# Optimization experiments

Measured on AMD Instinct MI355X. Metric: run time of the kernel, lower is better.

The kernel has to match this reference:

```python
import jax, jax.numpy as jnp
import numpy as np

B, T_ENC, T_DEC = 32, 300, 500
N_MEL, ENC_DIM, ATT_RNN, DEC_RNN, PRE = 80, 512, 1024, 1024, 256
ATT_DIM, LOC_F, LOC_K = 128, 32, 31
PAD = (LOC_K - 1) // 2
P_PRENET = 0.1


def _w(k, shape, fan_in):
    return jax.random.normal(k, shape, jnp.float32) / np.float32(np.sqrt(fan_in))


def setup_inputs() -> dict:
    key = jax.random.key(0)
    ks = jax.random.split(key, 20)
    lens = jax.random.randint(ks[2], (B,), T_ENC // 2, T_ENC + 1).at[0].set(T_ENC)
    return {
        "memory": jax.random.normal(ks[0], (B, T_ENC, ENC_DIM), jnp.float32),
        "decoder_inputs": jax.random.normal(ks[1], (B, N_MEL, T_DEC), jnp.float32),
        "memory_lengths": lens,
        "pre_W1": _w(ks[3], (PRE, N_MEL), N_MEL),
        "pre_W2": _w(ks[4], (PRE, PRE), PRE),
        "att_Wih": _w(ks[5], (4 * ATT_RNN, PRE + ENC_DIM), PRE + ENC_DIM),
        "att_Whh": _w(ks[6], (4 * ATT_RNN, ATT_RNN), ATT_RNN),
        "att_bih": jnp.zeros((4 * ATT_RNN,), jnp.float32),
        "att_bhh": jnp.zeros((4 * ATT_RNN,), jnp.float32),
        "q_W": _w(ks[7], (ATT_DIM, ATT_RNN), ATT_RNN),
        "m_W": _w(ks[8], (ATT_DIM, ENC_DIM), ENC_DIM),
        "v_w": _w(ks[9], (ATT_DIM,), ATT_DIM),
        "loc_conv_W": _w(ks[10], (LOC_F, 2, LOC_K), 2 * LOC_K),
        "loc_dense_W": _w(ks[11], (ATT_DIM, LOC_F), LOC_F),
        "dec_Wih": _w(ks[12], (4 * DEC_RNN, ATT_RNN + ENC_DIM), ATT_RNN + ENC_DIM),
        "dec_Whh": _w(ks[13], (4 * DEC_RNN, DEC_RNN), DEC_RNN),
        "dec_bih": jnp.zeros((4 * DEC_RNN,), jnp.float32),
        "dec_bhh": jnp.zeros((4 * DEC_RNN,), jnp.float32),
        "proj_W": _w(ks[14], (N_MEL, DEC_RNN + ENC_DIM), DEC_RNN + ENC_DIM),
        "proj_b": jnp.zeros((N_MEL,), jnp.float32),
        "gate_W": _w(ks[15], (DEC_RNN + ENC_DIM,), DEC_RNN + ENC_DIM),
        "gate_b": jnp.zeros((), jnp.float32),
    }


def _lstm(x, h, c, Wih, Whh, bih, bhh):
    # PyTorch LSTMCell gate order: i, f, g, o
    g = x @ Wih.T + bih + h @ Whh.T + bhh
    i, f, gg, o = jnp.split(g, 4, axis=-1)
    c = jax.nn.sigmoid(f) * c + jax.nn.sigmoid(i) * jnp.tanh(gg)
    h = jax.nn.sigmoid(o) * jnp.tanh(c)
    return h, c


def _prenet(x, W1, W2):
    # Original uses F.dropout(..., 0.1, training=True) always; deterministic masks here.
    k1, k2 = jax.random.split(jax.random.key(1))
    x = jax.nn.relu(x @ W1.T)
    x = x * jax.random.bernoulli(k1, 1.0 - P_PRENET, x.shape) / (1.0 - P_PRENET)
    x = jax.nn.relu(x @ W2.T)
    x = x * jax.random.bernoulli(k2, 1.0 - P_PRENET, x.shape) / (1.0 - P_PRENET)
    return x


def _forward(memory, decoder_inputs, memory_lengths, pre_W1, pre_W2, att_Wih, att_Whh,
             att_bih, att_bhh, q_W, m_W, v_w, loc_conv_W, loc_dense_W, dec_Wih, dec_Whh,
             dec_bih, dec_bhh, proj_W, proj_b, gate_W, gate_b):
    x = jnp.transpose(decoder_inputs, (2, 0, 1))          # [T_dec, B, n_mel]
    go = jnp.zeros((1,) + x.shape[1:], x.dtype)
    x = jnp.concatenate([go, x], axis=0)                  # [T_dec+1, B, n_mel]
    dec_ins = _prenet(x, pre_W1, pre_W2)[:-1]             # [T_dec, B, PRE]

    processed_memory = memory @ m_W.T                     # [B, T_enc, ATT_DIM]
    valid = jnp.arange(T_ENC)[None, :] < memory_lengths[:, None]  # [B, T_enc]
    Bn = memory.shape[0]
    zf = lambda d: jnp.zeros((Bn, d), memory.dtype)
    carry0 = (zf(ATT_RNN), zf(ATT_RNN), zf(DEC_RNN), zf(DEC_RNN),
              zf(T_ENC), zf(T_ENC), zf(ENC_DIM))

    def step(carry, x_t):
        ah, ac, dh, dc, aw, awc, ctx = carry
        ah, ac = _lstm(jnp.concatenate([x_t, ctx], 1), ah, ac,
                       att_Wih, att_Whh, att_bih, att_bhh)
        awcat = jnp.stack([aw, awc], axis=1)              # [B, 2, T_enc]
        loc = jax.lax.conv_general_dilated(awcat, loc_conv_W, (1,), [(PAD, PAD)],
                                           dimension_numbers=('NCH', 'OIH', 'NCH'))
        loc = jnp.transpose(loc, (0, 2, 1)) @ loc_dense_W.T   # [B, T_enc, ATT_DIM]
        pq = (ah @ q_W.T)[:, None, :]                     # [B, 1, ATT_DIM]
        e = jnp.tanh(pq + loc + processed_memory) @ v_w   # [B, T_enc]
        e = jnp.where(valid, e, -jnp.inf)
        aw = jax.nn.softmax(e, axis=1)
        ctx = jnp.einsum('bt,btd->bd', aw, memory)        # [B, ENC_DIM]
        awc = awc + aw
        dh, dc = _lstm(jnp.concatenate([ah, ctx], 1), dh, dc,
                       dec_Wih, dec_Whh, dec_bih, dec_bhh)
        dhac = jnp.concatenate([dh, ctx], 1)
        mel = dhac @ proj_W.T + proj_b                    # [B, n_mel]
        gate = dhac @ gate_W + gate_b                     # [B]
        return (ah, ac, dh, dc, aw, awc, ctx), (mel, gate, aw)

    _, (mels, gates, aligns) = jax.lax.scan(jax.checkpoint(step), carry0, dec_ins)
    mel_outputs = jnp.transpose(mels, (1, 2, 0))          # [B, n_mel, T_dec]
    gate_outputs = gates.T                                # [B, T_dec]
    alignments = jnp.transpose(aligns, (1, 0, 2))         # [B, T_dec, T_enc]
    return mel_outputs, gate_outputs, alignments


def reference(memory, decoder_inputs, memory_lengths, pre_W1, pre_W2, att_Wih, att_Whh,
              att_bih, att_bhh, q_W, m_W, v_w, loc_conv_W, loc_dense_W, dec_Wih, dec_Whh,
              dec_bih, dec_bhh, proj_W, proj_b, gate_W, gate_b):
    return _forward(memory, decoder_inputs, memory_lengths, pre_W1, pre_W2, att_Wih,
                    att_Whh, att_bih, att_bhh, q_W, m_W, v_w, loc_conv_W, loc_dense_W,
                    dec_Wih, dec_Whh, dec_bih, dec_bhh, proj_W, proj_b, gate_W, gate_b)
```

## Files before the change

kernel.cpp:

```cpp
#include <hip/hip_runtime.h>

#define NB 32
#define TENC 300
#define TDEC 500
#define NMEL 80
#define ENCD 512
#define PRE 256
#define ADIM 128
#define RD 4
#define WSPLIT 2944

#define OFF_DECINS 0ull
#define OFF_WHI    2048000ull
#define OFF_AHR    4096000ull
#define OFF_DHR    (OFF_AHR + 131072ull)
#define OFF_CXR    (OFF_DHR + 131072ull)
#define RINGS_N    327680ull
#define OFF_WLO    (OFF_AHR + RINGS_N)
#define OFF_PM     8192000ull
#define OFF_STATE  (OFF_PM + 1228800ull)
#define OFF_AC     (OFF_STATE + 0ull)
#define OFF_DC     (OFF_STATE + 32768ull)
#define OFF_AW     (OFF_STATE + 65536ull)
#define OFF_AWC    (OFF_STATE + 75136ull)
#define OFF_E      (OFF_STATE + 84736ull)
#define OFF_SLOTS  (OFF_STATE + 94336ull)
#define STATE_N    98440ull
#define OFF_QWT    (OFF_STATE + STATE_N)
#define OFF_PROJWT (OFF_QWT + 131072ull)
#define OFF_MWT    (OFF_PROJWT + 122880ull)
#define OFF_W1T    (OFF_MWT + 65536ull)
#define OFF_W2T    (OFF_W1T + 20480ull)

__device__ __forceinline__ unsigned short f2bf(float f){
  unsigned u = __float_as_uint(f);
  unsigned r = (u + 0x7FFFu + ((u >> 16) & 1u)) >> 16;
  return (unsigned short)r;
}
__device__ __forceinline__ float bf2f(unsigned short h){
  return __uint_as_float(((unsigned)h) << 16);
}

__device__ __forceinline__ float gload(const float* p){
  return __hip_atomic_load(p, __ATOMIC_RELAXED, __HIP_MEMORY_SCOPE_AGENT);
}
__device__ __forceinline__ void gstore(float* p, float v){
  __hip_atomic_store(p, v, __ATOMIC_RELAXED, __HIP_MEMORY_SCOPE_AGENT);
}

__device__ __forceinline__ void gbar(unsigned* slots, unsigned epoch){
  __syncthreads();
  int tid = threadIdx.x;
  if (tid == 0)
    __hip_atomic_store(&slots[blockIdx.x], epoch, __ATOMIC_RELAXED, __HIP_MEMORY_SCOPE_AGENT);
  if (tid < 64){
    const unsigned long long* p = (const unsigned long long*)slots;
    unsigned long long a, b;
    do {
      a = __hip_atomic_load(p + 2*tid,     __ATOMIC_RELAXED, __HIP_MEMORY_SCOPE_AGENT);
      b = __hip_atomic_load(p + 2*tid + 1, __ATOMIC_RELAXED, __HIP_MEMORY_SCOPE_AGENT);
    } while ((unsigned)a < epoch || (unsigned)(a >> 32) < epoch ||
             (unsigned)b < epoch || (unsigned)(b >> 32) < epoch);
  }
  __syncthreads();
}

__host__ __device__ __forceinline__ unsigned rotl32(unsigned v, int r){ return (v<<r)|(v>>(32-r)); }

__host__ __device__ __forceinline__ void tf2x32(unsigned k0, unsigned k1, unsigned c0, unsigned c1,
                                                unsigned& y0, unsigned& y1){
  unsigned ks2 = k0 ^ k1 ^ 0x1BD11BDAu;
  unsigned x0 = c0 + k0, x1 = c1 + k1;
#define TFR(r) x0 += x1; x1 = rotl32(x1, r); x1 ^= x0;
  TFR(13) TFR(15) TFR(26) TFR(6)
  x0 += k1;  x1 += ks2 + 1u;
  TFR(17) TFR(29) TFR(16) TFR(24)
  x0 += ks2; x1 += k0 + 2u;
  TFR(13) TFR(15) TFR(26) TFR(6)
  x0 += k0;  x1 += k1 + 3u;
  TFR(17) TFR(29) TFR(16) TFR(24)
  x0 += k1;  x1 += ks2 + 4u;
  TFR(13) TFR(15) TFR(26) TFR(6)
  x0 += ks2; x1 += k0 + 5u;
#undef TFR
  y0 = x0; y1 = x1;
}

__device__ __forceinline__ float mask_scale(unsigned k0, unsigned k1, unsigned idx){
  unsigned y0, y1;
  tf2x32(k0, k1, 0u, idx, y0, y1);
  unsigned bits = y0 ^ y1;
  float u = __uint_as_float((bits >> 9) | 0x3f800000u) - 1.0f;
  return (u < 0.9f) ? (1.0f/0.9f) : 0.0f;
}

__global__ __launch_bounds__(256) void k_setup(float* __restrict__ ws,
    const float* __restrict__ qW, const float* __restrict__ projW, const float* __restrict__ mW,
    const float* __restrict__ w1, const float* __restrict__ w2,
    const float* __restrict__ dWih, const float* __restrict__ dWhh){
  long i = (long)blockIdx.x*256 + threadIdx.x;
  long stride = (long)gridDim.x*256;
  float* st = ws + OFF_STATE;
  for (long x = i; x < (long)STATE_N; x += stride) st[x] = 0.f;
  float* qWT = ws + OFF_QWT;
  for (long x = i; x < 1024*128; x += stride){ int u = x>>7, d = x&127; qWT[x] = qW[(size_t)d*1024+u]; }
  float* pWT = ws + OFF_PROJWT;
  for (long x = i; x < 1536*80; x += stride){ int k = x/80, m = x%80; pWT[x] = projW[(size_t)m*1536+k]; }
  float* mWT = ws + OFF_MWT;
  for (long x = i; x < 512*128; x += stride){ int k = x>>7, d = x&127; mWT[x] = mW[(size_t)d*512+k]; }
  float* w1T = ws + OFF_W1T;
  for (long x = i; x < 80*256; x += stride){ int m = x>>8, u = x&255; w1T[x] = w1[(size_t)u*80+m]; }
  float* w2T = ws + OFF_W2T;
  for (long x = i; x < 256*256; x += stride){ int k = x>>8, u = x&255; w2T[x] = w2[(size_t)u*256+k]; }
  unsigned short* wlo = (unsigned short*)(ws + OFF_WLO);
  for (long x = i; x < (long)WSPLIT*2560; x += stride){
    int row = (int)(x/2560), c = (int)(x%2560);
    float v = (c < 1536) ? dWih[(size_t)row*1536 + c] : dWhh[(size_t)row*1024 + (c-1536)];
    wlo[x] = f2bf(v);
  }
  unsigned short* whi = (unsigned short*)(ws + OFF_WHI);
  for (long x = i; x < (long)(4096-WSPLIT)*2560; x += stride){
    int row = WSPLIT + (int)(x/2560), c = (int)(x%2560);
    float v = (c < 1536) ? dWih[(size_t)row*1536 + c] : dWhh[(size_t)row*1024 + (c-1536)];
    whi[x] = f2bf(v);
  }
}

__global__ __launch_bounds__(256) void k_prenet(const float* __restrict__ di,
    const float* __restrict__ W1T, const float* __restrict__ W2T,
    unsigned short* __restrict__ dec_ins,
    unsigned k10, unsigned k11, unsigned k20, unsigned k21){
  __shared__ float xs[NMEL];
  __shared__ float h1s[PRE];
  int bid = blockIdx.x;
  int t = bid >> 5, b = bid & 31;
  int tid = threadIdx.x;
  if (tid < NMEL) xs[tid] = (t == 0) ? 0.f : di[(size_t)b*40000 + (size_t)tid*500 + (t-1)];
  __syncthreads();
  float acc = 0.f;
  for (int m = 0; m < NMEL; ++m) acc += xs[m] * W1T[m*256 + tid];
  acc = fmaxf(acc, 0.f);
  unsigned idx = (unsigned)bid*256u + (unsigned)tid;
  h1s[tid] = acc * mask_scale(k10, k11, idx);
  __syncthreads();
  float a2 = 0.f;
  for (int k = 0; k < PRE; ++k) a2 += h1s[k] * W2T[k*256 + tid];
  a2 = fmaxf(a2, 0.f);
  a2 *= mask_scale(k20, k21, idx);
  dec_ins[(size_t)bid*256 + tid] = f2bf(a2);
}

__global__ __launch_bounds__(128) void k_procmem(const float* __restrict__ mem,
    const float* __restrict__ mWT, float* __restrict__ pm){
  __shared__ float ms[ENCD];
  int bid = blockIdx.x;
  int tid = threadIdx.x;
  const float* src = mem + (size_t)bid*ENCD;
  for (int i = tid; i < ENCD; i += 128) ms[i] = src[i];
  __syncthreads();
  float acc = 0.f;
  for (int k = 0; k < ENCD; ++k) acc += ms[k] * mWT[k*128 + tid];
  pm[(size_t)bid*128 + tid] = acc;
}

template<bool S0B>
__device__ __forceinline__ float2 xld2(const void* s0v, int l0, const float* s1,
                                       const float* h, int b, int k){
  if (k < l0){
    if constexpr (S0B){
      const unsigned short* s0 = (const unsigned short*)s0v;
      unsigned u = *(const unsigned*)(s0 + (size_t)b*l0 + k);
      float2 r; r.x = __uint_as_float((u & 0xFFFFu) << 16); r.y = __uint_as_float((u >> 16) << 16);
      return r;
    } else {
      const float* s0 = (const float*)s0v;
      return *(const float2*)(s0 + (size_t)b*l0 + k);
    }
  }
  if (k < l0 + 512) return *(const float2*)(s1 + (b<<9) + (k - l0));
  return *(const float2*)(h + (b<<10) + (k - (l0 + 512)));
}

template<bool S0B, bool WB>
__device__ __forceinline__ void lstm_block(int ub,
    const float* __restrict__ W1, const float* __restrict__ W2,
    const unsigned short* __restrict__ wlo, const unsigned short* __restrict__ whi,
    const float* __restrict__ bih, const float* __restrict__ bhh,
    const void* __restrict__ s0, int l0, const float* __restrict__ s1,
    const float* __restrict__ hprev, int Ktot,
    float* __restrict__ c_st, float* __restrict__ hnew, int tid){
  __shared__ float Xc[2][128*32];
  __shared__ float gates[16][32];
  const int xw = l0 + 512, xw4 = xw >> 2;
  const int NC = Ktot >> 7;
  const int w = tid >> 6, l = tid & 63;
  const int ss = l & 31, ph = l >> 5;
  const int rlA = 2*w, rlB = 2*w + 1;
  const int rowA = (rlA >> 2)*1024 + ub*4 + (rlA & 3);
  const int rowB = (rlB >> 2)*1024 + ub*4 + (rlB & 3);
  const float4* W1A = (const float4*)(W1 + (size_t)rowA*xw);
  const float4* W1B = (const float4*)(W1 + (size_t)rowB*xw);
  const float4* W2A = (const float4*)(W2 + ((size_t)rowA<<10));
  const float4* W2B = (const float4*)(W2 + ((size_t)rowB<<10));
  const unsigned short* BA = nullptr; const unsigned short* BB = nullptr;
  if constexpr (WB){
    BA = (rowA < WSPLIT) ? wlo + (size_t)rowA*2560 : whi + (size_t)(rowA - WSPLIT)*2560;
    BB = (rowB < WSPLIT) ? wlo + (size_t)rowB*2560 : whi + (size_t)(rowB - WSPLIT)*2560;
  }
  auto loadWA = [&](int f)->float4{
    if constexpr (WB){
      ushort4 h4 = *(const ushort4*)(BA + 4*(size_t)f);
      return make_float4(bf2f(h4.x), bf2f(h4.y), bf2f(h4.z), bf2f(h4.w));
    } else return (f < xw4) ? W1A[f] : W2A[f - xw4];
  };
  auto loadWB = [&](int f)->float4{
    if constexpr (WB){
      ushort4 h4 = *(const ushort4*)(BB + 4*(size_t)f);
      return make_float4(bf2f(h4.x), bf2f(h4.y), bf2f(h4.z), bf2f(h4.w));
    } else return (f < xw4) ? W1B[f] : W2B[f - xw4];
  };
  float accA[16] = {}, accB[16] = {};
  float2 sx[4];
#pragma unroll
  for (int it = 0; it < 4; ++it){
    int pidx = tid + it*512;
    int b = pidx >> 6, kL = (pidx & 63)*2;
    sx[it] = xld2<S0B>(s0, l0, s1, hprev, b, kL);
  }
#pragma unroll
  for (int it = 0; it < 4; ++it){
    int pidx = tid + it*512;
    int b = pidx >> 6, kL = (pidx & 63)*2;
    int a0 = kL*32 + (((b>>2) ^ ((kL>>2)&7))<<2) + (b&3);
    Xc[0][a0] = sx[it].x; Xc[0][a0+32] = sx[it].y;
  }
  float4 wA = loadWA(ss), wB = loadWB(ss);
  __syncthreads();

  for (int c = 0; c < NC; ++c){
    float4 wAn, wBn;
    if (c + 1 < NC){
      int f = (c+1)*32 + ss;
      wAn = loadWA(f); wBn = loadWB(f);
      int kg0 = (c+1) << 7;
#pragma unroll
      for (int it = 0; it < 4; ++it){
        int pidx = tid + it*512;
        int b = pidx >> 6, kL = (pidx & 63)*2;
        sx[it] = xld2<S0B>(s0, l0, s1, hprev, b, kg0 + kL);
      }
    }
    const float4* X4 = (const float4*)Xc[c & 1];
    const int sw = ss & 7;
#pragma unroll
    for (int e = 0; e < 4; ++e){
      int kL = 4*ss + e;
      float ea = (e==0)?wA.x:(e==1)?wA.y:(e==2)?wA.z:wA.w;
      float eb = (e==0)?wB.x:(e==1)?wB.y:(e==2)?wB.z:wB.w;
      int base = kL*8;
#pragma unroll
      for (int j = 0; j < 4; ++j){
        int g = ph*4 + j;
        float4 xv = X4[base + (g ^ sw)];
        accA[4*j+0] += ea*xv.x; accA[4*j+1] += ea*xv.y;
        accA[4*j+2] += ea*xv.z; accA[4*j+3] += ea*xv.w;
        accB[4*j+0] += eb*xv.x; accB[4*j+1] += eb*xv.y;
        accB[4*j+2] += eb*xv.z; accB[4*j+3] += eb*xv.w;
      }
    }
    if (c + 1 < NC){
#pragma unroll
      for (int it = 0; it < 4; ++it){
        int pidx = tid + it*512;
        int b = pidx >> 6, kL = (pidx & 63)*2;
        int a0 = kL*32 + (((b>>2) ^ ((kL>>2)&7))<<2) + (b&3);
        Xc[(c+1)&1][a0] = sx[it].x; Xc[(c+1)&1][a0+32] = sx[it].y;
      }
      wA = wAn; wB = wBn;
    }
    __syncthreads();
  }
#pragma unroll
  for (int j = 0; j < 16; ++j){
    accA[j] += __shfl_xor(accA[j], 16, 64);
    accB[j] += __shfl_xor(accB[j], 16, 64);
  }
#pragma unroll
  for (int m = 8; m >= 1; m >>= 1){
    int up = ss & m;
#pragma unroll
    for (int j = 0; j < m; ++j){
      float sA = up ? accA[j] : accA[j+m];
      float kA = up ? accA[j+m] : accA[j];
      float sB = up ? accB[j] : accB[j+m];
      float kB = up ? accB[j+m] : accB[j];
      accA[j] = kA + __shfl_xor(sA, m, 64);
      accB[j] = kB + __shfl_xor(sB, m, 64);
    }
  }
  if (!(l & 16)){
    int b = ph*16 + (l & 15);
    gates[rlA][b] = accA[0];
    gates[rlB][b] = accB[0];
  }
  __syncthreads();
  if (tid < 128){
    int b = tid & 31, u = tid >> 5;
    int gu = ub*4 + u;
    float gi = gates[u][b]     + bih[gu]         + bhh[gu];
    float gf = gates[4+u][b]   + bih[1024+gu]    + bhh[1024+gu];
    float gg = gates[8+u][b]   + bih[2048+gu]    + bhh[2048+gu];
    float go = gates[12+u][b]  + bih[3072+gu]    + bhh[3072+gu];
    float ii = 1.f/(1.f + expf(-gi));
    float ff = 1.f/(1.f + expf(-gf));
    float oo = 1.f/(1.f + expf(-go));
    float tg = tanhf(gg);
    float cold = gload(&c_st[b*1024 + gu]);
    float cn = ff*cold + ii*tg;
    gstore(&c_st[b*1024 + gu], cn);
    gstore(&hnew[b*1024 + gu], oo*tanhf(cn));
  }
  __syncthreads();
}

__device__ __forceinline__ void energy_tile(int b, int tile, bool act, int h,
    const float* __restrict__ aw, const float* __restrict__ awc,
    const float* __restrict__ lcW, const float* __restrict__ ldW, const float* __restrict__ vw,
    const float* __restrict__ sPq, const float* __restrict__ pm, float* __restrict__ e_ws, int t2){
  __shared__ float sIn[2][2][46];
  __shared__ float cfs[2][16][33];
  __shared__ float ep[2][16][17];
  int j0 = tile*16;
  if (act){
    if (t2 < 46){ int j = j0 - 15 + t2; sIn[h][0][t2] = (j >= 0 && j < 300) ? gload(&aw[b*300 + j]) : 0.f; }
    else if (t2 < 92){ int i = t2 - 46; int j = j0 - 15 + i; sIn[h][1][i] = (j >= 0 && j < 300) ? gload(&awc[b*300 + j]) : 0.f; }
  }
  __syncthreads();
  if (act){
    int fg = t2 & 15, jl = t2 >> 4;
    int f0 = 2*fg;
    float c0 = 0.f, c1 = 0.f;
#pragma unroll
    for (int c = 0; c < 2; ++c)
#pragma unroll
      for (int k = 0; k < 31; ++k){
        float a = sIn[h][c][jl + k];
        c0 += a * lcW[f0*62 + c*31 + k];
        c1 += a * lcW[(f0+1)*62 + c*31 + k];
      }
    cfs[h][jl][f0] = c0; cfs[h][jl][f0+1] = c1;
  }
  __syncthreads();
  if (act){
    int dg = t2 & 15, jl = t2 >> 4;
    int j = j0 + jl;
    float s = 0.f;
    if (j < 300){
      const float* pmrow = pm + ((size_t)(b*300 + j))*128 + dg*8;
#pragma unroll
      for (int dd = 0; dd < 8; ++dd){
        int d = dg*8 + dd;
        float acc = sPq[d] + pmrow[dd];
#pragma unroll
        for (int f = 0; f < 32; ++f) acc += cfs[h][jl][f] * ldW[d*32 + f];
        s += vw[d] * tanhf(acc);
      }
    }
    ep[h][jl][dg] = s;
  }
  __syncthreads();
  if (act && t2 < 16){
    int j = j0 + t2;
    if (j < 300){
      float s = 0.f;
#pragma unroll
      for (int dg = 0; dg < 16; ++dg) s += ep[h][t2][dg];
      gstore(&e_ws[b*300 + j], s);
    }
  }
  __syncthreads();
}

__device__ __forceinline__ void pq_energy(int b, int jt, const float* __restrict__ ah,
    const float* __restrict__ qWT, const float* __restrict__ aw, const float* __restrict__ awc,
    const float* __restrict__ lcW, const float* __restrict__ ldW, const float* __restrict__ vw,
    const float* __restrict__ pm, float* __restrict__ e_ws, int tid){
  __shared__ float sAh[1024];
  __shared__ float pqs[512];
  __shared__ float sPq[128];
  for (int i = tid; i < 1024; i += 512) sAh[i] = ah[b*1024 + i];
  __syncthreads();
  int d = tid & 127, seg = tid >> 7;
  const float* qt = qWT + (size_t)(seg*256)*128 + d;
  const float* sh = sAh + seg*256;
  float a0 = 0.f, a1 = 0.f, a2 = 0.f, a3 = 0.f;
  for (int u = 0; u < 256; u += 4){
    a0 += sh[u]   * qt[(size_t)u*128];
    a1 += sh[u+1] * qt[(size_t)(u+1)*128];
    a2 += sh[u+2] * qt[(size_t)(u+2)*128];
    a3 += sh[u+3] * qt[(size_t)(u+3)*128];
  }
  pqs[seg*128 + d] = (a0 + a1) + (a2 + a3);
  __syncthreads();
  if (tid < 128) sPq[tid] = (pqs[tid] + pqs[128+tid]) + (pqs[256+tid] + pqs[384+tid]);
  __syncthreads();
  int h = tid >> 8, t2 = tid & 255;
  for (int r = 0; r < 2; ++r){
    int tile = r*16 + jt*2 + h;
    energy_tile(b, tile, tile < 19, h, aw, awc, lcW, ldW, vw, sPq, pm, e_ws, t2);
  }
}

__device__ __forceinline__ void dec_out_slice(int b, int jt,
    const float* __restrict__ dh, const float* __restrict__ ctx,
    const float* __restrict__ pWT, const float* __restrict__ projb,
    const float* __restrict__ gateW, const float* __restrict__ gateb,
    float* __restrict__ out, int s, int tid){
  __shared__ float sX[1536];
  __shared__ float melp[48][11];
  __shared__ float gatep[32];
  for (int i = tid; i < 1024; i += 512) sX[i] = dh[b*1024 + i];
  if (tid < 512) { int i = tid; sX[1024 + i] = ctx[b*512 + i]; }
  __syncthreads();
  if (tid < 480){
    int mi = tid % 10, kseg = tid / 10;
    int m = jt*10 + mi;
    const float* pw = pWT + m;
    int k0 = kseg*32;
    float a0 = 0.f, a1 = 0.f;
#pragma unroll 8
    for (int k = 0; k < 32; k += 2){
      a0 += sX[k0+k]   * pw[(size_t)(k0+k)*80];
      a1 += sX[k0+k+1] * pw[(size_t)(k0+k+1)*80];
    }
    melp[kseg][mi] = a0 + a1;
  } else if (jt == 0){
    int kseg = tid - 480;
    int k0 = kseg*48;
    float a = 0.f;
    for (int k = 0; k < 48; ++k) a += sX[k0+k] * gateW[k0+k];
    gatep[kseg] = a;
  }
  __syncthreads();
  if (tid < 10){
    float s2 = projb[jt*10 + tid];
    for (int q = 0; q < 48; ++q) s2 += melp[q][tid];
    out[(size_t)b*40000 + (size_t)(jt*10 + tid)*500 + s] = s2;
  }
  if (jt == 0 && tid == 10){
    float s2 = gateb[0];
    for (int q = 0; q < 32; ++q) s2 += gatep[q];
    out[1280000 + (size_t)b*500 + s] = s2;
  }
  __syncthreads();
}

__device__ __forceinline__ void soft_phase(int b, int dsl, const float* __restrict__ e_ws,
    const int* __restrict__ lens, const float* __restrict__ mem,
    float* __restrict__ aw, float* __restrict__ awc, float* __restrict__ ctx,
    float* __restrict__ out, int t, int tid){
  __shared__ float se[300];
  __shared__ float sa[300];
  __shared__ float red[512];
  int len = lens[b];
  for (int j = tid; j < 300; j += 512) se[j] = gload(&e_ws[b*300 + j]);
  __syncthreads();
  float m = -1e30f;
  for (int j = tid; j < len; j += 512) m = fmaxf(m, se[j]);
  red[tid] = m; __syncthreads();
  for (int s = 256; s > 0; s >>= 1){ if (tid < s) red[tid] = fmaxf(red[tid], red[tid + s]); __syncthreads(); }
  float mx = red[0]; __syncthreads();
  float ssum = 0.f;
  for (int j = tid; j < len; j += 512) ssum += expf(se[j] - mx);
  red[tid] = ssum; __syncthreads();
  for (int s = 256; s > 0; s >>= 1){ if (tid < s) red[tid] += red[tid + s]; __syncthreads(); }
  float inv = 1.f/red[0];
  __syncthreads();
  float* al = out + 1296000 + (size_t)b*150000 + (size_t)t*300;
  for (int j = tid; j < 300; j += 512){
    float v = (j < len) ? expf(se[j] - mx)*inv : 0.f;
    sa[j] = v;
    if (dsl == 0){
      gstore(&aw[b*300 + j], v);
      gstore(&awc[b*300 + j], gload(&awc[b*300 + j]) + v);
      al[j] = v;
    }
  }
  __syncthreads();
  int d = dsl*64 + (tid & 63), jq = tid >> 6;
  int chunk = (len + 7) >> 3;
  int j0 = jq*chunk, j1 = min(len, j0 + chunk);
  float a0 = 0.f, a1 = 0.f;
  const float* mb = mem + (size_t)b*153600 + d;
  int j = j0;
  for (; j + 1 < j1; j += 2){
    a0 += sa[j]   * mb[(size_t)j*512];
    a1 += sa[j+1] * mb[(size_t)(j+1)*512];
  }
  if (j < j1) a0 += sa[j]*mb[(size_t)j*512];
  red[tid] = a0 + a1; __syncthreads();
  if (jq == 0){
    int ln = tid & 63;
    float s = 0.f;
#pragma unroll
    for (int q = 0; q < 8; ++q) s += red[ln + 64*q];
    gstore(&ctx[b*512 + d], s);
  }
  __syncthreads();
}

struct DecParams {
  const float *memory;
  const int   *lens;
  const float *attWih, *attWhh, *attBih, *attBhh;
  const float *decBih, *decBhh;
  const float *lcW, *ldW, *vw, *projb, *gateW, *gateb;
  float *ws, *out;
};

__global__ void __launch_bounds__(512, 2) k_loop(DecParams p){
  int wg = blockIdx.x, tid = threadIdx.x;
  float* ws = p.ws;
  const unsigned short* decins = (const unsigned short*)(ws + OFF_DECINS);
  const unsigned short* wlo = (const unsigned short*)(ws + OFF_WLO);
  const unsigned short* whi = (const unsigned short*)(ws + OFF_WHI);
  float* e_ws = ws + OFF_E;
  float* pm = ws + OFF_PM;
  float* AC = ws + OFF_AC;
  float* DC = ws + OFF_DC;
  float* aw = ws + OFF_AW;
  float* awc = ws + OFF_AWC;
  float* qWT = ws + OFF_QWT;
  float* pWT = ws + OFF_PROJWT;
  unsigned* slots = (unsigned*)(ws + OFF_SLOTS);
  unsigned ep = 0;
  int b = wg >> 3, jt = wg & 7;

#define AHR(s) (ws + OFF_AHR + (size_t)(s)*32768)
#define DHR(s) (ws + OFF_DHR + (size_t)(s)*32768)
#define CXR(s) (ws + OFF_CXR + (size_t)(s)*16384)

  for (unsigned i = (unsigned)wg*512u + tid; i < (unsigned)RINGS_N; i += 131072u)
    gstore(ws + OFF_AHR + i, 0.f);
  gbar(slots, ++ep);

  lstm_block<true,false>(wg, p.attWih, p.attWhh, nullptr, nullptr, p.attBih, p.attBhh,
                         decins, PRE, CXR(0), AHR(0), 1792, AC, AHR(1), tid);
  gbar(slots, ++ep);

  for (int t = 0; t < TDEC; ++t){
    int cu = (t + 1) % RD, pr = t % RD, nx = (t + 2) % RD;
    pq_energy(b, jt, AHR(cu), qWT, aw, awc, p.lcW, p.ldW, p.vw, pm, e_ws, tid);
    if (t > 0)
      dec_out_slice(b, jt, DHR(pr), CXR(pr), pWT, p.projb, p.gateW, p.gateb, p.out, t - 1, tid);
    gbar(slots, ++ep);
    soft_phase(b, jt, e_ws, p.lens, p.memory, aw, awc, CXR(cu), p.out, t, tid);
    gbar(slots, ++ep);
    lstm_block<false,true>(wg, nullptr, nullptr, wlo, whi, p.decBih, p.decBhh,
                           AHR(cu), 1024, CXR(cu), DHR(pr), 2560, DC, DHR(cu), tid);
    if (t + 1 < TDEC)
      lstm_block<true,false>(wg, p.attWih, p.attWhh, nullptr, nullptr, p.attBih, p.attBhh,
                             decins + (size_t)(t + 1)*NB*PRE, PRE, CXR(cu), AHR(cu), 1792,
                             AC, AHR(nx), tid);
    gbar(slots, ++ep);
  }
  dec_out_slice(b, jt, DHR(500 % RD), CXR(500 % RD), pWT, p.projb, p.gateW, p.gateb,
                p.out, TDEC - 1, tid);
#undef AHR
#undef DHR
#undef CXR
}

extern "C" void kernel_launch(void* const* d_in, const int* in_sizes, int n_in,
                              void* d_out, int out_size, void* d_ws, size_t ws_size,
                              hipStream_t stream) {
  const float* memory   = (const float*)d_in[0];
  const float* dec_in   = (const float*)d_in[1];
  const int*   lens     = (const int*)  d_in[2];
  const float* pre_W1   = (const float*)d_in[3];
  const float* pre_W2   = (const float*)d_in[4];
  const float* att_Wih  = (const float*)d_in[5];
  const float* att_Whh  = (const float*)d_in[6];
  const float* att_bih  = (const float*)d_in[7];
  const float* att_bhh  = (const float*)d_in[8];
  const float* q_W      = (const float*)d_in[9];
  const float* m_W      = (const float*)d_in[10];
  const float* v_w      = (const float*)d_in[11];
  const float* lc_W     = (const float*)d_in[12];
  const float* ld_W     = (const float*)d_in[13];
  const float* dec_Wih  = (const float*)d_in[14];
  const float* dec_Whh  = (const float*)d_in[15];
  const float* dec_bih  = (const float*)d_in[16];
  const float* dec_bhh  = (const float*)d_in[17];
  const float* proj_W   = (const float*)d_in[18];
  const float* proj_b   = (const float*)d_in[19];
  const float* gate_W   = (const float*)d_in[20];
  const float* gate_b   = (const float*)d_in[21];
  float* out = (float*)d_out;
  float* ws  = (float*)d_ws;

  unsigned k10, k11, k20, k21;
  tf2x32(0u, 1u, 0u, 0u, k10, k11);
  tf2x32(0u, 1u, 0u, 1u, k20, k21);

  k_setup<<<1024, 256, 0, stream>>>(ws, q_W, proj_W, m_W, pre_W1, pre_W2, dec_Wih, dec_Whh);
  k_prenet<<<TDEC*NB, 256, 0, stream>>>(dec_in, ws + OFF_W1T, ws + OFF_W2T,
                                        (unsigned short*)(ws + OFF_DECINS), k10, k11, k20, k21);
  k_procmem<<<NB*TENC, 128, 0, stream>>>(memory, ws + OFF_MWT, ws + OFF_PM);

  DecParams hp;
  hp.memory = memory; hp.lens = lens;
  hp.attWih = att_Wih; hp.attWhh = att_Whh; hp.attBih = att_bih; hp.attBhh = att_bhh;
  hp.decBih = dec_bih; hp.decBhh = dec_bhh;
  hp.lcW = lc_W; hp.ldW = ld_W; hp.vw = v_w; hp.projb = proj_b; hp.gateW = gate_W; hp.gateb = gate_b;
  hp.ws = ws; hp.out = out;
  k_loop<<<256, 512, 0, stream>>>(hp);
}
```

Before: 77.00 ms.

## Compute full attention energies per block redundantly to drop a grid barrier

Each of the 8 workgroups per batch row now computes all 19 energy tiles itself, rather than its own slice exchanged through global memory. Softmax, the attention-weight state and the cumulative weights are kept in shared memory, so the e_ws/aw/awc global buffers and one grid-wide barrier per decoder step are removed. The cost is 8x redundant location-conv and energy work per batch row, and extra LDS use that may affect occupancy.

```diff
diff --git a/kernel.cpp b/kernel.cpp
--- a/kernel.cpp
+++ b/kernel.cpp
@@ -21,11 +21,8 @@
 #define OFF_STATE  (OFF_PM + 1228800ull)
 #define OFF_AC     (OFF_STATE + 0ull)
 #define OFF_DC     (OFF_STATE + 32768ull)
-#define OFF_AW     (OFF_STATE + 65536ull)
-#define OFF_AWC    (OFF_STATE + 75136ull)
-#define OFF_E      (OFF_STATE + 84736ull)
-#define OFF_SLOTS  (OFF_STATE + 94336ull)
-#define STATE_N    98440ull
+#define OFF_SLOTS  (OFF_STATE + 65536ull)
+#define STATE_N    65600ull
 #define OFF_QWT    (OFF_STATE + STATE_N)
 #define OFF_PROJWT (OFF_QWT + 131072ull)
 #define OFF_MWT    (OFF_PROJWT + 122880ull)
@@ -323,17 +320,18 @@
   __syncthreads();
 }
 
-__device__ __forceinline__ void energy_tile(int b, int tile, bool act, int h,
-    const float* __restrict__ aw, const float* __restrict__ awc,
+__device__ __forceinline__ void energy_tile_l(float* __restrict__ se,
+    const float* __restrict__ saw, const float* __restrict__ sawc,
+    int tile, bool act, int h,
     const float* __restrict__ lcW, const float* __restrict__ ldW, const float* __restrict__ vw,
-    const float* __restrict__ sPq, const float* __restrict__ pm, float* __restrict__ e_ws, int t2){
+    const float* __restrict__ sPq, const float* __restrict__ pmb, int t2){
   __shared__ float sIn[2][2][46];
   __shared__ float cfs[2][16][33];
   __shared__ float ep[2][16][17];
   int j0 = tile*16;
   if (act){
-    if (t2 < 46){ int j = j0 - 15 + t2; sIn[h][0][t2] = (j >= 0 && j < 300) ? gload(&aw[b*300 + j]) : 0.f; }
-    else if (t2 < 92){ int i = t2 - 46; int j = j0 - 15 + i; sIn[h][1][i] = (j >= 0 && j < 300) ? gload(&awc[b*300 + j]) : 0.f; }
+    if (t2 < 46){ int j = j0 - 15 + t2; sIn[h][0][t2] = (j >= 0 && j < 300) ? saw[j] : 0.f; }
+    else if (t2 < 92){ int i = t2 - 46; int j = j0 - 15 + i; sIn[h][1][i] = (j >= 0 && j < 300) ? sawc[j] : 0.f; }
   }
   __syncthreads();
   if (act){
@@ -356,7 +354,7 @@
     int j = j0 + jl;
     float s = 0.f;
     if (j < 300){
-      const float* pmrow = pm + ((size_t)(b*300 + j))*128 + dg*8;
+      const float* pmrow = pmb + (size_t)j*128 + dg*8;
 #pragma unroll
       for (int dd = 0; dd < 8; ++dd){
         int d = dg*8 + dd;
@@ -375,40 +373,85 @@
       float s = 0.f;
 #pragma unroll
       for (int dg = 0; dg < 16; ++dg) s += ep[h][t2][dg];
-      gstore(&e_ws[b*300 + j], s);
-    }
-  }
-  __syncthreads();
-}
-
-__device__ __forceinline__ void pq_energy(int b, int jt, const float* __restrict__ ah,
-    const float* __restrict__ qWT, const float* __restrict__ aw, const float* __restrict__ awc,
+      se[j] = s;
+    }
+  }
+  __syncthreads();
+}
+
+__device__ __forceinline__ void bphase(int b, int jt, const float* __restrict__ ah,
+    const float* __restrict__ qWT, float* __restrict__ saw, float* __restrict__ sawc,
     const float* __restrict__ lcW, const float* __restrict__ ldW, const float* __restrict__ vw,
-    const float* __restrict__ pm, float* __restrict__ e_ws, int tid){
+    const float* __restrict__ pm, const int* __restrict__ lens, const float* __restrict__ mem,
+    float* __restrict__ ctx, float* __restrict__ out, int t, int tid){
   __shared__ float sAh[1024];
   __shared__ float pqs[512];
   __shared__ float sPq[128];
+  __shared__ float se[304];
+  __shared__ float red[512];
   for (int i = tid; i < 1024; i += 512) sAh[i] = ah[b*1024 + i];
   __syncthreads();
-  int d = tid & 127, seg = tid >> 7;
-  const float* qt = qWT + (size_t)(seg*256)*128 + d;
-  const float* sh = sAh + seg*256;
-  float a0 = 0.f, a1 = 0.f, a2 = 0.f, a3 = 0.f;
-  for (int u = 0; u < 256; u += 4){
-    a0 += sh[u]   * qt[(size_t)u*128];
-    a1 += sh[u+1] * qt[(size_t)(u+1)*128];
-    a2 += sh[u+2] * qt[(size_t)(u+2)*128];
-    a3 += sh[u+3] * qt[(size_t)(u+3)*128];
-  }
-  pqs[seg*128 + d] = (a0 + a1) + (a2 + a3);
+  {
+    int d = tid & 127, seg = tid >> 7;
+    const float* qt = qWT + (size_t)(seg*256)*128 + d;
+    const float* sh = sAh + seg*256;
+    float a0 = 0.f, a1 = 0.f, a2 = 0.f, a3 = 0.f;
+    for (int u = 0; u < 256; u += 4){
+      a0 += sh[u]   * qt[(size_t)u*128];
+      a1 += sh[u+1] * qt[(size_t)(u+1)*128];
+      a2 += sh[u+2] * qt[(size_t)(u+2)*128];
+      a3 += sh[u+3] * qt[(size_t)(u+3)*128];
+    }
+    pqs[seg*128 + d] = (a0 + a1) + (a2 + a3);
+  }
   __syncthreads();
   if (tid < 128) sPq[tid] = (pqs[tid] + pqs[128+tid]) + (pqs[256+tid] + pqs[384+tid]);
   __syncthreads();
+  const float* pmb = pm + (size_t)b*300*128;
   int h = tid >> 8, t2 = tid & 255;
-  for (int r = 0; r < 2; ++r){
-    int tile = r*16 + jt*2 + h;
-    energy_tile(b, tile, tile < 19, h, aw, awc, lcW, ldW, vw, sPq, pm, e_ws, t2);
-  }
+  for (int r = 0; r < 10; ++r){
+    int tile = r*2 + h;
+    energy_tile_l(se, saw, sawc, tile, tile < 19, h, lcW, ldW, vw, sPq, pmb, t2);
+  }
+  int len = lens[b];
+  float m = -1e30f;
+  for (int j = tid; j < len; j += 512) m = fmaxf(m, se[j]);
+  red[tid] = m; __syncthreads();
+  for (int s = 256; s > 0; s >>= 1){ if (tid < s) red[tid] = fmaxf(red[tid], red[tid + s]); __syncthreads(); }
+  float mx = red[0]; __syncthreads();
+  float ssum = 0.f;
+  for (int j = tid; j < len; j += 512) ssum += expf(se[j] - mx);
+  red[tid] = ssum; __syncthreads();
+  for (int s = 256; s > 0; s >>= 1){ if (tid < s) red[tid] += red[tid + s]; __syncthreads(); }
+  float inv = 1.f/red[0];
+  __syncthreads();
+  float* al = out + 1296000 + (size_t)b*150000 + (size_t)t*300;
+  for (int j = tid; j < 300; j += 512){
+    float v = (j < len) ? expf(se[j] - mx)*inv : 0.f;
+    se[j] = v; saw[j] = v; sawc[j] += v;
+    if (jt == 0) al[j] = v;
+  }
+  __syncthreads();
+  int d = jt*64 + (tid & 63), jq = tid >> 6;
+  int chunk = (len + 7) >> 3;
+  int j0 = jq*chunk, j1 = min(len, j0 + chunk);
+  float a0 = 0.f, a1 = 0.f;
+  const float* mb = mem + (size_t)b*153600 + d;
+  int j = j0;
+  for (; j + 1 < j1; j += 2){
+    a0 += se[j]   * mb[(size_t)j*512];
+    a1 += se[j+1] * mb[(size_t)(j+1)*512];
+  }
+  if (j < j1) a0 += se[j]*mb[(size_t)j*512];
+  red[tid] = a0 + a1; __syncthreads();
+  if (jq == 0){
+    int ln = tid & 63;
+    float s = 0.f;
+#pragma unroll
+    for (int q = 0; q < 8; ++q) s += red[ln + 64*q];
+    gstore(&ctx[b*512 + d], s);
+  }
+  __syncthreads();
 }
 
 __device__ __forceinline__ void dec_out_slice(int b, int jt,
@@ -455,60 +498,6 @@
   __syncthreads();
 }
 
-__device__ __forceinline__ void soft_phase(int b, int dsl, const float* __restrict__ e_ws,
-    const int* __restrict__ lens, const float* __restrict__ mem,
-    float* __restrict__ aw, float* __restrict__ awc, float* __restrict__ ctx,
-    float* __restrict__ out, int t, int tid){
-  __shared__ float se[300];
-  __shared__ float sa[300];
-  __shared__ float red[512];
-  int len = lens[b];
-  for (int j = tid; j < 300; j += 512) se[j] = gload(&e_ws[b*300 + j]);
-  __syncthreads();
-  float m = -1e30f;
-  for (int j = tid; j < len; j += 512) m = fmaxf(m, se[j]);
-  red[tid] = m; __syncthreads();
-  for (int s = 256; s > 0; s >>= 1){ if (tid < s) red[tid] = fmaxf(red[tid], red[tid + s]); __syncthreads(); }
-  float mx = red[0]; __syncthreads();
-  float ssum = 0.f;
-  for (int j = tid; j < len; j += 512) ssum += expf(se[j] - mx);
-  red[tid] = ssum; __syncthreads();
-  for (int s = 256; s > 0; s >>= 1){ if (tid < s) red[tid] += red[tid + s]; __syncthreads(); }
-  float inv = 1.f/red[0];
-  __syncthreads();
-  float* al = out + 1296000 + (size_t)b*150000 + (size_t)t*300;
-  for (int j = tid; j < 300; j += 512){
-    float v = (j < len) ? expf(se[j] - mx)*inv : 0.f;
-    sa[j] = v;
-    if (dsl == 0){
-      gstore(&aw[b*300 + j], v);
-      gstore(&awc[b*300 + j], gload(&awc[b*300 + j]) + v);
-      al[j] = v;
-    }
-  }
-  __syncthreads();
-  int d = dsl*64 + (tid & 63), jq = tid >> 6;
-  int chunk = (len + 7) >> 3;
-  int j0 = jq*chunk, j1 = min(len, j0 + chunk);
-  float a0 = 0.f, a1 = 0.f;
-  const float* mb = mem + (size_t)b*153600 + d;
-  int j = j0;
-  for (; j + 1 < j1; j += 2){
-    a0 += sa[j]   * mb[(size_t)j*512];
-    a1 += sa[j+1] * mb[(size_t)(j+1)*512];
-  }
-  if (j < j1) a0 += sa[j]*mb[(size_t)j*512];
-  red[tid] = a0 + a1; __syncthreads();
-  if (jq == 0){
-    int ln = tid & 63;
-    float s = 0.f;
-#pragma unroll
-    for (int q = 0; q < 8; ++q) s += red[ln + 64*q];
-    gstore(&ctx[b*512 + d], s);
-  }
-  __syncthreads();
-}
-
 struct DecParams {
   const float *memory;
   const int   *lens;
@@ -519,22 +508,22 @@
 };
 
 __global__ void __launch_bounds__(512, 2) k_loop(DecParams p){
+  __shared__ float saw[304];
+  __shared__ float sawc[304];
   int wg = blockIdx.x, tid = threadIdx.x;
   float* ws = p.ws;
   const unsigned short* decins = (const unsigned short*)(ws + OFF_DECINS);
   const unsigned short* wlo = (const unsigned short*)(ws + OFF_WLO);
   const unsigned short* whi = (const unsigned short*)(ws + OFF_WHI);
-  float* e_ws = ws + OFF_E;
   float* pm = ws + OFF_PM;
   float* AC = ws + OFF_AC;
   float* DC = ws + OFF_DC;
-  float* aw = ws + OFF_AW;
-  float* awc = ws + OFF_AWC;
   float* qWT = ws + OFF_QWT;
   float* pWT = ws + OFF_PROJWT;
   unsigned* slots = (unsigned*)(ws + OFF_SLOTS);
   unsigned ep = 0;
   int b = wg >> 3, jt = wg & 7;
+  for (int i = tid; i < 304; i += 512){ saw[i] = 0.f; sawc[i] = 0.f; }
 
 #define AHR(s) (ws + OFF_AHR + (size_t)(s)*32768)
 #define DHR(s) (ws + OFF_DHR + (size_t)(s)*32768)
@@ -550,11 +539,10 @@
 
   for (int t = 0; t < TDEC; ++t){
     int cu = (t + 1) % RD, pr = t % RD, nx = (t + 2) % RD;
-    pq_energy(b, jt, AHR(cu), qWT, aw, awc, p.lcW, p.ldW, p.vw, pm, e_ws, tid);
+    bphase(b, jt, AHR(cu), qWT, saw, sawc, p.lcW, p.ldW, p.vw, pm, p.lens, p.memory,
+           CXR(cu), p.out, t, tid);
     if (t > 0)
       dec_out_slice(b, jt, DHR(pr), CXR(pr), pWT, p.projb, p.gateW, p.gateb, p.out, t - 1, tid);
-    gbar(slots, ++ep);
-    soft_phase(b, jt, e_ws, p.lens, p.memory, aw, awc, CXR(cu), p.out, t, tid);
     gbar(slots, ++ep);
     lstm_block<false,true>(wg, nullptr, nullptr, wlo, whi, p.decBih, p.decBhh,
                            AHR(cu), 1024, CXR(cu), DHR(pr), 2560, DC, DHR(cu), tid);
```

Result: slower. 151.7 ms (+97.0%).
